# Performance work log

Hardware: AMD Instinct MI355X
Metric: run time of the kernel (lower is better)

## Reference

```python
import jax, jax.numpy as jnp
import numpy as np

# ImageNet normalization constants (as used by watermark-anything's normalize_img/unnormalize_img)
_MEAN = jnp.array([0.485, 0.456, 0.406], dtype=jnp.float32).reshape(1, 3, 1, 1)
_STD = jnp.array([0.229, 0.224, 0.225], dtype=jnp.float32).reshape(1, 3, 1, 1)


def unnormalize_img(x):
    return x * _STD + _MEAN


def normalize_img(x):
    return (x - _MEAN) / _STD


def median_filter(img, k):
    # img: [B, C, H, W]; k: static odd python int
    pad = k // 2
    B, C, H, W = img.shape
    xp = jnp.pad(img, ((0, 0), (0, 0), (pad, pad), (pad, pad)), mode='reflect')
    # Gather k*k shifted views (small fixed loop over window offsets, not data dims)
    wins = [xp[:, :, i:i + H, j:j + W] for i in range(k) for j in range(k)]
    stack = jnp.stack(wins, axis=-1)  # [B, C, H, W, k*k]
    # k*k is odd -> jnp.median == torch.median (exact middle order statistic)
    return jnp.median(stack, axis=-1)


def setup_inputs() -> dict:
    key = jax.random.key(0)
    k1, k2 = jax.random.split(key)
    image = jax.random.normal(k1, (8, 3, 512, 512), dtype=jnp.float32)
    mask = jax.random.uniform(k2, (8, 1, 512, 512), dtype=jnp.float32)
    return {"image": image, "mask": mask, "kernel_size": 7}


def reference(image, mask, kernel_size):
    img = jnp.clip(unnormalize_img(image), 0.0, 1.0)
    med = median_filter(img, kernel_size)
    # passthrough=True: straight-through estimator
    out = jax.lax.stop_gradient(med - img) + img
    return (normalize_img(out), mask)
```

## Files before the change

### kernel.cpp

```cpp
#include <hip/hip_runtime.h>
#include <stdint.h>


#define TW 32
#define TH 16
#define LW (TW + 6)
#define LHK 22
#define LHP 26
#define HW 512

typedef unsigned short u16x2 __attribute__((ext_vector_type(2)));

__device__ __forceinline__ void ce(uint32_t &a, uint32_t &b) {
  u16x2 av = __builtin_bit_cast(u16x2, a);
  u16x2 bv = __builtin_bit_cast(u16x2, b);
  u16x2 lo = __builtin_elementwise_min(av, bv);
  u16x2 hi = __builtin_elementwise_max(av, bv);
  a = __builtin_bit_cast(uint32_t, lo);
  b = __builtin_bit_cast(uint32_t, hi);
}

template<int L, int P>
__device__ __forceinline__ void bitonic_merge(uint32_t *buf) {
#pragma unroll
  for (int s = L >> 1; s >= 1; s >>= 1) {
#pragma unroll
    for (int i = 0; i < L; ++i) {
      if (((i & s) == 0) && i >= P)
        ce(buf[i], buf[i + s]);
    }
  }
}

template<int M, int N>
__device__ __forceinline__ void merge2(const uint32_t *a, const uint32_t *b, uint32_t *out) {
  constexpr int T = M + N;
  constexpr int L = (T <= 2) ? 2 : (T <= 4) ? 4 : (T <= 8) ? 8 : (T <= 16) ? 16 : (T <= 32) ? 32 : 64;
  constexpr int P = L - T;
  uint32_t buf[L];
#pragma unroll
  for (int i = 0; i < M; ++i) buf[P + i] = a[i];
#pragma unroll
  for (int i = 0; i < N; ++i) buf[P + M + i] = b[N - 1 - i];
  bitonic_merge<L, P>(buf);
#pragma unroll
  for (int i = 0; i < T; ++i) out[i] = buf[P + i];
}

__device__ __forceinline__ uint32_t f32_key(float f) {
  union { float f; uint32_t u; } cv; cv.f = f;
  uint32_t u = cv.u;
  uint32_t h = (u + 0x7FFFu + ((u >> 16) & 1u)) >> 16;
  h &= 0xFFFFu;
  return (h & 0x8000u) ? (~h & 0xFFFFu) : (h | 0x8000u);
}

__device__ __forceinline__ float key_to_f32(uint32_t k) {
  uint32_t h = (k & 0x8000u) ? (k ^ 0x8000u) : (~k & 0xFFFFu);
  union { uint32_t u; float f; } cv; cv.u = h << 16;
  return cv.f;
}

__global__ __launch_bounds__(256) void fused_kernel(
    const float* __restrict__ img, const float* __restrict__ mask,
    float* __restrict__ out) {
  if (blockIdx.z >= 24) {
    int flat = (((int)(blockIdx.z - 24) * gridDim.y + blockIdx.y) * gridDim.x + blockIdx.x) * 256
               + threadIdx.x;
    const float4* s = (const float4*)mask;
    float4* d = (float4*)(out + (size_t)8 * 3 * HW * HW);
    d[flat] = s[flat];
    return;
  }

  __shared__ uint16_t keyT[LW][LHP];
  __shared__ uint32_t scol[8][7][LW];

  const int tx = threadIdx.x & (TW - 1);
  const int ty = threadIdx.x >> 5;
  const int bx = blockIdx.x * TW;
  const int by = blockIdx.y * TH;
  const int z  = blockIdx.z;
  const size_t base = (size_t)z * (HW * HW);
  const float* src = img + base;

  for (int idx = threadIdx.x; idx < LHK * LW; idx += 256) {
    int r = idx / LW, cc = idx - r * LW;
    int gy = by - 3 + r;
    int gx = bx - 3 + cc;
    gy = (gy < 0) ? -gy : ((gy >= HW) ? (2 * HW - 2 - gy) : gy);
    gx = (gx < 0) ? -gx : ((gx >= HW) ? (2 * HW - 2 - gx) : gx);
    keyT[cc][r] = (uint16_t)f32_key(src[gy * HW + gx]);
  }
  __syncthreads();

  for (int cidx = threadIdx.x; cidx < 8 * LW; cidx += 256) {
    int y0 = cidx & 7, x = cidx >> 3;
    const uint32_t* colp = (const uint32_t*)&keyT[x][2 * y0];
    uint32_t w0 = colp[0], w1 = colp[1], w2 = colp[2], w3 = colp[3];
    uint32_t col[7];
    col[0] = w0; col[2] = w1; col[4] = w2; col[6] = w3;
    col[1] = __builtin_amdgcn_alignbit(w1, w0, 16);
    col[3] = __builtin_amdgcn_alignbit(w2, w1, 16);
    col[5] = __builtin_amdgcn_alignbit(w3, w2, 16);
#pragma unroll
    for (int a = 1; a < 7; ++a)
#pragma unroll
      for (int b = a; b > 0; --b)
        ce(col[b - 1], col[b]);
#pragma unroll
    for (int e = 0; e < 7; ++e)
      scol[y0][e][x] = col[e];
  }
  __syncthreads();

  uint32_t c[7][7];
  {
    const uint32_t* sbase = &scol[ty][0][tx];
#pragma unroll
    for (int j = 0; j < 7; ++j)
#pragma unroll
      for (int e = 0; e < 7; ++e)
        c[j][e] = sbase[e * LW + j];
  }

  uint32_t p01[14], p23[14], p45[14];
  merge2<7, 7>(c[0], c[1], p01);
  merge2<7, 7>(c[2], c[3], p23);
  merge2<7, 7>(c[4], c[5], p45);
  uint32_t s03[28];
  merge2<14, 14>(p01, p23, s03);
  uint32_t t46[21];
  merge2<14, 7>(p45, c[6], t46);

  uint32_t buf[64];
#pragma unroll
  for (int i = 0; i < 22; ++i) buf[21 + i] = s03[3 + i];
#pragma unroll
  for (int i = 0; i < 21; ++i) buf[43 + i] = t46[20 - i];

#pragma unroll
  for (int i = 21; i < 32; ++i) ce(buf[i], buf[i + 32]);
#pragma unroll
  for (int i = 32; i < 48; ++i) ce(buf[i], buf[i + 16]);
#pragma unroll
  for (int i = 32; i < 40; ++i) ce(buf[i], buf[i + 8]);
#pragma unroll
  for (int i = 40; i < 44; ++i) ce(buf[i], buf[i + 4]);
  ce(buf[40], buf[42]); ce(buf[41], buf[43]);
  ce(buf[42], buf[43]);
  uint32_t med = buf[42];

  const int ch = z - (z / 3) * 3;
  float mean, stdv;
  if (ch == 0)      { mean = 0.485f; stdv = 0.229f; }
  else if (ch == 1) { mean = 0.456f; stdv = 0.224f; }
  else              { mean = 0.406f; stdv = 0.225f; }

  float m[2];
  m[0] = key_to_f32(med & 0xFFFFu);
  m[1] = key_to_f32(med >> 16);
#pragma unroll
  for (int p = 0; p < 2; ++p) {
    float y = __fadd_rn(__fmul_rn(m[p], stdv), mean);
    y = fminf(fmaxf(y, 0.0f), 1.0f);
    y = __fdiv_rn(__fsub_rn(y, mean), stdv);
    out[base + (size_t)(by + 2 * ty + p) * HW + (bx + tx)] = y;
  }
}

extern "C" void kernel_launch(void* const* d_in, const int* in_sizes, int n_in,
                              void* d_out, int out_size, void* d_ws, size_t ws_size,
                              hipStream_t stream) {
  const float* img  = (const float*)d_in[0];
  const float* mask = (const float*)d_in[1];
  float* out = (float*)d_out;

  dim3 grid(HW / TW, HW / TH, 24 + 4);
  fused_kernel<<<grid, 256, 0, stream>>>(img, mask, out);
}
```

Before: 132.4 us.

## Share pairwise column merges across threads through LDS

Adjacent sorted 7-element columns are now merged once per column pair by the whole block and stored in a new shared buffer. Each thread then reads three precomputed 14-element runs plus one column, instead of doing three 7+7 bitonic merges itself. This removes duplicated sorting work between neighbouring output pixels. In exchange it adds about 16KB of shared memory, an extra barrier, and an uneven 288-task loop over 256 threads, which may reduce occupancy.

```diff
diff --git a/kernel.cpp b/kernel.cpp
--- a/kernel.cpp
+++ b/kernel.cpp
@@ -7,6 +7,7 @@
 #define LW (TW + 6)
 #define LHK 22
 #define LHP 26
+#define NP 36
 #define HW 512
 
 typedef unsigned short u16x2 __attribute__((ext_vector_type(2)));
@@ -75,6 +76,7 @@
 
   __shared__ uint16_t keyT[LW][LHP];
   __shared__ uint32_t scol[8][7][LW];
+  __shared__ uint32_t pairm[8][14][NP];
 
   const int tx = threadIdx.x & (TW - 1);
   const int ty = threadIdx.x >> 5;
@@ -114,24 +116,34 @@
   }
   __syncthreads();
 
-  uint32_t c[7][7];
-  {
-    const uint32_t* sbase = &scol[ty][0][tx];
+  for (int pidx = threadIdx.x; pidx < 8 * NP; pidx += 256) {
+    int y0 = pidx & 7, p = pidx >> 3;
+    uint32_t a[7], b[7];
 #pragma unroll
-    for (int j = 0; j < 7; ++j)
+    for (int e = 0; e < 7; ++e) { a[e] = scol[y0][e][p]; b[e] = scol[y0][e][p + 1]; }
+    uint32_t m[14];
+    merge2<7, 7>(a, b, m);
 #pragma unroll
-      for (int e = 0; e < 7; ++e)
-        c[j][e] = sbase[e * LW + j];
+    for (int e = 0; e < 14; ++e)
+      pairm[y0][e][p] = m[e];
   }
+  __syncthreads();
 
-  uint32_t p01[14], p23[14], p45[14];
-  merge2<7, 7>(c[0], c[1], p01);
-  merge2<7, 7>(c[2], c[3], p23);
-  merge2<7, 7>(c[4], c[5], p45);
+  uint32_t A[14], B[14], C[14], D[7];
+#pragma unroll
+  for (int e = 0; e < 14; ++e) {
+    A[e] = pairm[ty][e][tx];
+    B[e] = pairm[ty][e][tx + 2];
+    C[e] = pairm[ty][e][tx + 4];
+  }
+#pragma unroll
+  for (int e = 0; e < 7; ++e)
+    D[e] = scol[ty][e][tx + 6];
+
   uint32_t s03[28];
-  merge2<14, 14>(p01, p23, s03);
+  merge2<14, 14>(A, B, s03);
   uint32_t t46[21];
-  merge2<14, 7>(p45, c[6], t46);
+  merge2<14, 7>(C, D, t46);
 
   uint32_t buf[64];
 #pragma unroll
@@ -157,12 +169,12 @@
   else if (ch == 1) { mean = 0.456f; stdv = 0.224f; }
   else              { mean = 0.406f; stdv = 0.225f; }
 
-  float m[2];
-  m[0] = key_to_f32(med & 0xFFFFu);
-  m[1] = key_to_f32(med >> 16);
+  float m0 = key_to_f32(med & 0xFFFFu);
+  float m1 = key_to_f32(med >> 16);
+  float mm[2] = {m0, m1};
 #pragma unroll
   for (int p = 0; p < 2; ++p) {
-    float y = __fadd_rn(__fmul_rn(m[p], stdv), mean);
+    float y = __fadd_rn(__fmul_rn(mm[p], stdv), mean);
     y = fminf(fmaxf(y, 0.0f), 1.0f);
     y = __fdiv_rn(__fsub_rn(y, mean), stdv);
     out[base + (size_t)(by + 2 * ty + p) * HW + (bx + tx)] = y;
```

New measurement: 132.3 us. Within noise of the previous version (-0.0%).
